# Kernel tuning notes

Measured on AMD Instinct MI355X. Metric: run time of the kernel, lower is better.

Reference implementation:

```python
import jax, jax.numpy as jnp
import numpy as np

EMBED_DIM = 1024
NUM_HEADS = 16
HEAD_DIM = EMBED_DIM // NUM_HEADS


def setup_inputs() -> dict:
    key = jax.random.key(0)
    ks = jax.random.split(key, 6)
    std = 0.02
    x = jax.random.normal(ks[0], (2, 2048, EMBED_DIM), dtype=jnp.float32)
    Wq = jax.random.normal(ks[1], (EMBED_DIM, EMBED_DIM), dtype=jnp.float32) * std
    Wk = jax.random.normal(ks[2], (EMBED_DIM, EMBED_DIM), dtype=jnp.float32) * std
    Wv = jax.random.normal(ks[3], (EMBED_DIM, EMBED_DIM), dtype=jnp.float32) * std
    Wo = jax.random.normal(ks[4], (EMBED_DIM, EMBED_DIM), dtype=jnp.float32) * std
    Wf = jax.random.normal(ks[5], (NUM_HEADS, EMBED_DIM), dtype=jnp.float32) * std
    return {"x": x, "Wq": Wq, "Wk": Wk, "Wv": Wv, "Wo": Wo, "Wf": Wf}


def reference(x, Wq, Wk, Wv, Wo, Wf):
    b, n, d = x.shape
    h, hd = NUM_HEADS, HEAD_DIM
    # projections (nn.Linear without bias: y = x @ W^T)
    q = (x @ Wq.T).reshape(b, n, h, hd)
    k = (x @ Wk.T).reshape(b, n, h, hd)
    v = (x @ Wv.T).reshape(b, n, h, hd)
    # per-head log forget gate and its causal cumulative sum
    log_f = jax.nn.log_sigmoid(x @ Wf.T)          # [b, n, h]
    c = jnp.cumsum(log_f, axis=1)                 # [b, n, h], c_i = sum_{t<=i} log f_t
    cbh = c.transpose(0, 2, 1)                    # [b, h, n]
    scale = 1.0 / np.sqrt(hd).astype(np.float32)
    # scores s_ij = q_i.k_j * scale + (c_i - c_j)  (decay D_ij = sum_{t=j+1}^i log f_t)
    scores = jnp.einsum("bihd,bjhd->bhij", q, k) * scale
    scores = scores + cbh[:, :, :, None] - cbh[:, :, None, :]
    causal = jnp.tril(jnp.ones((n, n), dtype=bool))
    scores = jnp.where(causal, scores, -1e30)
    p = jax.nn.softmax(scores, axis=-1)           # [b, h, n, n]
    out = jnp.einsum("bhij,bjhd->bihd", p, v).reshape(b, n, d)
    return out @ Wo.T
```

## Files before the change

### kernel.cpp

```cpp
#include <hip/hip_runtime.h>

#define EMBED 1024
#define NHEAD 16
#define HD    64
#define SEQ   2048
#define BATCH 2
#define ROWS  (BATCH * SEQ)

typedef float f32x4 __attribute__((ext_vector_type(4)));
typedef short short8 __attribute__((ext_vector_type(8)));
typedef short short4v __attribute__((ext_vector_type(4)));
typedef unsigned short u16x4 __attribute__((ext_vector_type(4)));
typedef unsigned short u16x8 __attribute__((ext_vector_type(8)));
typedef unsigned u32x4 __attribute__((ext_vector_type(4)));
typedef unsigned u32x2 __attribute__((ext_vector_type(2)));

#define LOG2E 1.4426950408889634f

__device__ __forceinline__ unsigned short f2bf(float f) {
  unsigned int u = __builtin_bit_cast(unsigned int, f);
  u += 0x7fffu + ((u >> 16) & 1u);
  return (unsigned short)(u >> 16);
}

__device__ __forceinline__ unsigned cvtpk(float lo, float hi) {
  unsigned r;
  asm("v_cvt_pk_bf16_f32 %0, %1, %2" : "=v"(r) : "v"(lo), "v"(hi));
  return r;
}

#if __has_builtin(__builtin_amdgcn_exp2f)
#define EXP2(x) __builtin_amdgcn_exp2f(x)
#else
#define EXP2(x) exp2f(x)
#endif

__device__ __forceinline__ void gll16(const void* g, const void* l) {
  __builtin_amdgcn_global_load_lds(
      (const __attribute__((address_space(1))) unsigned int*)g,
      (__attribute__((address_space(3))) unsigned int*)l, 16, 0, 0);
}

__device__ __forceinline__ unsigned lds_addr(const void* p) {
  return (unsigned)(size_t)(__attribute__((address_space(3))) const void*)p;
}

__global__ __launch_bounds__(256) void cvt_all_kernel(
    const float* __restrict__ x,
    const float* __restrict__ w0, const float* __restrict__ w1,
    const float* __restrict__ w2, const float* __restrict__ w3,
    const float* __restrict__ wf,
    unsigned short* __restrict__ xo,
    unsigned short* __restrict__ o0, unsigned short* __restrict__ o1,
    unsigned short* __restrict__ o2, unsigned short* __restrict__ o3,
    unsigned short* __restrict__ wfh, unsigned short* __restrict__ wfl,
    unsigned* __restrict__ qkmaxu) {
  const int y = blockIdx.y;
  if (y < 4) {
    const float* in = (y == 0) ? w0 : (y == 1) ? w1 : (y == 2) ? w2 : w3;
    unsigned short* out = (y == 0) ? o0 : (y == 1) ? o1 : (y == 2) ? o2 : o3;
    const int i = blockIdx.x * 256 + threadIdx.x;
    f32x4 v = reinterpret_cast<const f32x4*>(in)[i];
    u16x4 o;
#pragma unroll
    for (int e = 0; e < 4; ++e) o[e] = f2bf(v[e]);
    reinterpret_cast<u16x4*>(out)[i] = o;
  } else if (y == 4) {
    const int i0 = blockIdx.x * 256 + threadIdx.x;
#pragma unroll
    for (int e = 0; e < 4; ++e) {
      const int i = i0 + e * 262144;
      f32x4 v = reinterpret_cast<const f32x4*>(x)[i];
      u16x4 h;
#pragma unroll
      for (int q = 0; q < 4; ++q) h[q] = f2bf(v[q]);
      reinterpret_cast<u16x4*>(xo)[i] = h;
    }
  } else {
    if (blockIdx.x < 16) {
      const int i = blockIdx.x * 256 + threadIdx.x;
      f32x4 v = reinterpret_cast<const f32x4*>(wf)[i];
      u16x4 h, l;
#pragma unroll
      for (int q = 0; q < 4; ++q) {
        h[q] = f2bf(v[q]);
        const float hf = __builtin_bit_cast(float, (unsigned)h[q] << 16);
        l[q] = f2bf(v[q] - hf);
      }
      reinterpret_cast<u16x4*>(wfh)[i] = h;
      reinterpret_cast<u16x4*>(wfl)[i] = l;
    } else if (blockIdx.x == 16) {
      if (threadIdx.x < 64) qkmaxu[threadIdx.x] = 0u;
    }
  }
}

__global__ __launch_bounds__(256) void gemm_wo_kernel(
    const unsigned short* __restrict__ A, const unsigned short* __restrict__ B,
    float* __restrict__ C) {
  __shared__ unsigned short Asm[64 * 64];
  __shared__ unsigned short Bsm[128 * 64];
  const int tid = threadIdx.x, wid = tid >> 6, lane = tid & 63;
  const int g = lane >> 4, l16 = lane & 15;
  const int wr = wid >> 1, wc = wid & 1;
  const int mb = blockIdx.y;
  const int nb = blockIdx.x;

  f32x4 acc[2][4] = {};

  for (int k0 = 0; k0 < EMBED; k0 += 64) {
    __syncthreads();
#pragma unroll
    for (int q = 0; q < 2; ++q) {
      const int base = (wid * 2 + q) * 1024;
      const int off = base + lane * 16;
      const int row = off >> 7;
      const int colel = (off & 127) >> 1;
      gll16(A + (size_t)(mb * 64 + row) * EMBED + k0 + colel, (const char*)Asm + base);
    }
#pragma unroll
    for (int q = 0; q < 4; ++q) {
      const int base = (wid * 4 + q) * 1024;
      const int off = base + lane * 16;
      const int row = off >> 7;
      const int colel = (off & 127) >> 1;
      gll16(B + (size_t)(nb * 128 + row) * EMBED + k0 + colel, (const char*)Bsm + base);
    }
    __syncthreads();

#pragma unroll
    for (int kc = 0; kc < 2; ++kc) {
      short8 am[2], bm[4];
#pragma unroll
      for (int mi = 0; mi < 2; ++mi)
        am[mi] = *reinterpret_cast<const short8*>(&Asm[(wr * 32 + mi * 16 + l16) * 64 + kc * 32 + g * 8]);
#pragma unroll
      for (int ni = 0; ni < 4; ++ni)
        bm[ni] = *reinterpret_cast<const short8*>(&Bsm[(wc * 64 + ni * 16 + l16) * 64 + kc * 32 + g * 8]);
#pragma unroll
      for (int mi = 0; mi < 2; ++mi)
#pragma unroll
        for (int ni = 0; ni < 4; ++ni)
          acc[mi][ni] = __builtin_amdgcn_mfma_f32_16x16x32_bf16(am[mi], bm[ni], acc[mi][ni], 0, 0, 0);
    }
  }

#pragma unroll
  for (int mi = 0; mi < 2; ++mi)
#pragma unroll
    for (int ni = 0; ni < 4; ++ni)
#pragma unroll
      for (int r = 0; r < 4; ++r) {
        const int m = mb * 64 + wr * 32 + mi * 16 + g * 4 + r;
        const int n = nb * 128 + wc * 64 + ni * 16 + l16;
        C[(size_t)m * EMBED + n] = acc[mi][ni][r];
      }
}

#define BAR() asm volatile("s_barrier" ::: "memory")
#define LGKM0()                                              \
  do {                                                       \
    asm volatile("s_waitcnt lgkmcnt(0)" ::: "memory");       \
    __builtin_amdgcn_sched_barrier(0);                       \
  } while (0)
#define VM(n_) asm volatile("s_waitcnt vmcnt(" #n_ ")" ::: "memory")

template <bool OUT_BF16>
__global__ __launch_bounds__(512, 2) void gemm256_kernel(
    const unsigned short* __restrict__ A,
    const unsigned short* __restrict__ B0, const unsigned short* __restrict__ B1,
    const unsigned short* __restrict__ B2,
    void* __restrict__ C0, void* __restrict__ C1, void* __restrict__ C2,
    unsigned* __restrict__ qkmaxu) {
  __shared__ unsigned short sm[2][2][2][8192];
  const int tid = threadIdx.x, wid = tid >> 6, lane = tid & 63;
  const int g = lane >> 4, l16 = lane & 15;
  const int wr = wid >> 2, wcol = wid & 3;
  const int mb = blockIdx.y;
  const int nb = blockIdx.x;
  const int which = nb >> 2;
  const int col0 = (nb & 3) * 256;
  const unsigned short* Bp = (which == 0) ? B0 : (which == 1) ? B1 : B2;
  void* Cp = (which == 0) ? C0 : (which == 1) ? C1 : C2;

  const int lane8 = lane & 7, laneHi = lane >> 3;
  const int colel = (lane8 ^ laneHi) * 8;
  int soff[2];
#pragma unroll
  for (int q = 0; q < 2; ++q)
    soff[q] = (q * 64 + wid * 8 + laneHi) * EMBED + colel;
  const unsigned short* Ag = A + (size_t)(mb * 256) * EMBED;
  const unsigned short* Bg = Bp + (size_t)col0 * EMBED;

  const int sw = (l16 & 7) << 4;
  const int cs0 = (0 | (g * 16)) ^ sw;
  const int cs1 = (64 | (g * 16)) ^ sw;
  const char* smB = (const char*)sm;
  const int aBase = wr * 16384 + l16 * 128;
  const int bBase = 32768 + (wcol >> 1) * 16384 + (wcol & 1) * 8192 + l16 * 128;

#define STG(buf_, ab_, half_, gsrc_, t_)                                               \
  do {                                                                                 \
    const unsigned short* gp_ = (gsrc_) + (size_t)(half_) * (128 * EMBED) + (t_) * 64; \
    char* lp_ = (char*)sm + (buf_) * 65536 + (ab_) * 32768 + (half_) * 16384 + wid * 1024; \
    gll16(gp_ + soff[0], lp_);                                                         \
    gll16(gp_ + soff[1], lp_ + 8192);                                                  \
  } while (0)

#define RD_A(buf_, row_, kc_) \
  (*reinterpret_cast<const short8*>(smB + (buf_) * 65536 + aBase + (row_) * 2048 + ((kc_) ? cs1 : cs0)))
#define RD_B(buf_, row_, kc_) \
  (*reinterpret_cast<const short8*>(smB + (buf_) * 65536 + bBase + (row_) * 2048 + ((kc_) ? cs1 : cs0)))

#define QUAD(mg_, ng_)                                                                   \
  do {                                                                                   \
    __builtin_amdgcn_s_setprio(1);                                                       \
    _Pragma("unroll") for (int kc_ = 0; kc_ < 2; ++kc_)                                  \
      _Pragma("unroll") for (int mi_ = 0; mi_ < 4; ++mi_)                                \
        _Pragma("unroll") for (int nj_ = 0; nj_ < 2; ++nj_)                              \
          acc[(mg_) * 4 + mi_][(ng_) * 2 + nj_] = __builtin_amdgcn_mfma_f32_16x16x32_bf16( \
              fa[mi_][kc_], fb[(ng_) * 2 + nj_][kc_], acc[(mg_) * 4 + mi_][(ng_) * 2 + nj_], 0, 0, 0); \
    __builtin_amdgcn_s_setprio(0);                                                       \
  } while (0)

#define KTILE4(BUF_, STG_P1, STG_P2, STG_P3, STG_P4_VM)                                  \
  do {                                                                                   \
    _Pragma("unroll") for (int mi_ = 0; mi_ < 4; ++mi_) {                                \
      fa[mi_][0] = RD_A(BUF_, mi_, 0);                                                   \
      fa[mi_][1] = RD_A(BUF_, mi_, 1);                                                   \
    }                                                                                    \
    _Pragma("unroll") for (int ni_ = 0; ni_ < 2; ++ni_) {                                \
      fb[ni_][0] = RD_B(BUF_, ni_, 0);                                                   \
      fb[ni_][1] = RD_B(BUF_, ni_, 1);                                                   \
    }                                                                                    \
    STG_P1;                                                                              \
    asm volatile("s_waitcnt lgkmcnt(8)" ::: "memory");                                   \
    BAR();                                                                               \
    LGKM0();                                                                             \
    QUAD(0, 0);                                                                          \
    BAR();                                                                               \
    _Pragma("unroll") for (int ni_ = 0; ni_ < 2; ++ni_) {                                \
      fb[2 + ni_][0] = RD_B(BUF_, 2 + ni_, 0);                                           \
      fb[2 + ni_][1] = RD_B(BUF_, 2 + ni_, 1);                                           \
    }                                                                                    \
    STG_P2;                                                                              \
    BAR();                                                                               \
    LGKM0();                                                                             \
    QUAD(0, 1);                                                                          \
    BAR();                                                                               \
    _Pragma("unroll") for (int mi_ = 0; mi_ < 4; ++mi_) {                                \
      fa[mi_][0] = RD_A(BUF_, 4 + mi_, 0);                                               \
      fa[mi_][1] = RD_A(BUF_, 4 + mi_, 1);                                               \
    }                                                                                    \
    STG_P3;                                                                              \
    BAR();                                                                               \
    LGKM0();                                                                             \
    QUAD(1, 0);                                                                          \
    BAR();                                                                               \
    STG_P4_VM;                                                                           \
    BAR();                                                                               \
    QUAD(1, 1);                                                                          \
    BAR();                                                                               \
  } while (0)

  short8 fa[4][2], fb[4][2];
  f32x4 acc[8][4] = {};

  STG(0, 0, 0, Ag, 0);
  STG(0, 1, 0, Bg, 0);
  STG(0, 0, 1, Ag, 0);
  STG(0, 1, 1, Bg, 0);
  STG(1, 1, 0, Bg, 1);
  STG(1, 1, 1, Bg, 1);
  VM(4);
  BAR();

  for (int it = 0; it < 8; ++it) {
    const int t1 = 2 * it + 1, t2 = 2 * it + 2, t3 = 2 * it + 3;
    const bool nl = (it < 7);
    KTILE4(0,
           STG(1, 0, 0, Ag, t1),
           STG(1, 0, 1, Ag, t1),
           if (nl) STG(0, 1, 0, Bg, t2),
           if (nl) { STG(0, 1, 1, Bg, t2); VM(4); } else VM(0));
    KTILE4(1,
           if (nl) STG(0, 0, 0, Ag, t2),
           if (nl) STG(0, 0, 1, Ag, t2),
           if (nl) STG(1, 1, 0, Bg, t3),
           if (nl) { STG(1, 1, 1, Bg, t3); VM(4); });
  }

  unsigned mxv = 0;
#pragma unroll
  for (int mi = 0; mi < 8; ++mi)
#pragma unroll
    for (int ni = 0; ni < 4; ++ni)
#pragma unroll
      for (int r = 0; r < 4; ++r) {
        const int m = mb * 256 + wr * 128 + mi * 16 + g * 4 + r;
        const int n = col0 + wcol * 64 + ni * 16 + l16;
        if (OUT_BF16) {
          const unsigned short bv = f2bf(acc[mi][ni][r]);
          ((unsigned short*)Cp)[(size_t)m * EMBED + n] = bv;
          const unsigned a = bv & 0x7fffu;
          mxv = a > mxv ? a : mxv;
        } else {
          ((float*)Cp)[(size_t)m * EMBED + n] = acc[mi][ni][r];
        }
      }
  if (OUT_BF16 && which < 2) {
#pragma unroll
    for (int mm = 1; mm < 64; mm <<= 1) {
      const unsigned o = __shfl_xor(mxv, mm);
      mxv = o > mxv ? o : mxv;
    }
    if (lane == 0) {
      const int bbat = (mb >= 8) ? 1 : 0;
      const int head = (nb & 3) * 4 + wcol;
      const int idx = which * 32 + bbat * 16 + head;
      atomicMax(&qkmaxu[idx], mxv << 16);
    }
  }
#undef STG
#undef RD_A
#undef RD_B
#undef QUAD
#undef KTILE4
}
#undef BAR
#undef LGKM0
#undef VM

__global__ __launch_bounds__(256) void gate_kernel(
    const float* __restrict__ x,
    const unsigned short* __restrict__ wh, const unsigned short* __restrict__ wl,
    float* __restrict__ c) {
  __shared__ f32x4 red[4][64];
  const int tid = threadIdx.x, wid = tid >> 6, lane = tid & 63;
  const int g = lane >> 4, l16 = lane & 15;
  const int row0 = blockIdx.x * 16;
  const int k0 = wid * 256;
  const float* xp = x + (size_t)(row0 + l16) * EMBED + k0 + g * 8;
  const unsigned short* whp = wh + (size_t)l16 * EMBED + k0 + g * 8;
  const unsigned short* wlp = wl + (size_t)l16 * EMBED + k0 + g * 8;
  f32x4 acc = {};
#pragma unroll
  for (int k = 0; k < 8; ++k) {
    const f32x4 v0 = *reinterpret_cast<const f32x4*>(xp + k * 32);
    const f32x4 v1 = *reinterpret_cast<const f32x4*>(xp + k * 32 + 4);
    short8 ah, al;
#pragma unroll
    for (int e = 0; e < 4; ++e) {
      const unsigned short h0 = f2bf(v0[e]);
      ah[e] = (short)h0;
      al[e] = (short)f2bf(v0[e] - __builtin_bit_cast(float, (unsigned)h0 << 16));
      const unsigned short h1 = f2bf(v1[e]);
      ah[e + 4] = (short)h1;
      al[e + 4] = (short)f2bf(v1[e] - __builtin_bit_cast(float, (unsigned)h1 << 16));
    }
    const short8 bh = *reinterpret_cast<const short8*>(whp + k * 32);
    const short8 bl = *reinterpret_cast<const short8*>(wlp + k * 32);
    acc = __builtin_amdgcn_mfma_f32_16x16x32_bf16(ah, bh, acc, 0, 0, 0);
    acc = __builtin_amdgcn_mfma_f32_16x16x32_bf16(ah, bl, acc, 0, 0, 0);
    acc = __builtin_amdgcn_mfma_f32_16x16x32_bf16(al, bh, acc, 0, 0, 0);
  }
  red[wid][lane] = acc;
  __syncthreads();
  if (wid == 0) {
    const f32x4 a = red[0][lane] + red[1][lane] + red[2][lane] + red[3][lane];
#pragma unroll
    for (int r = 0; r < 4; ++r) {
      const float s = a[r];
      const float ls = (fminf(s, 0.f) - log1pf(__expf(-fabsf(s)))) * LOG2E;
      const int n = row0 + g * 4 + r;
      const int b = n >> 11, nn = n & (SEQ - 1);
      c[(size_t)(b * NHEAD + l16) * SEQ + nn] = ls;
    }
  }
}

__global__ void cumsum_kernel(float* __restrict__ c) {
  const int bh = blockIdx.x;
  const int lane = threadIdx.x;
  float* p = c + (size_t)bh * SEQ;
  f32x4 vv[8];
  f32x4* vp = reinterpret_cast<f32x4*>(p + lane * 32);
#pragma unroll
  for (int q = 0; q < 8; ++q) vv[q] = vp[q];
  float run = 0.f;
#pragma unroll
  for (int q = 0; q < 8; ++q)
#pragma unroll
    for (int e = 0; e < 4; ++e) { run += vv[q][e]; vv[q][e] = run; }
  float s = run;
#pragma unroll
  for (int off = 1; off < 64; off <<= 1) {
    float u = __shfl_up(s, off);
    if (lane >= off) s += u;
  }
  const float excl = s - run;
#pragma unroll
  for (int q = 0; q < 8; ++q)
#pragma unroll
    for (int e = 0; e < 4; ++e) vv[q][e] += excl;
#pragma unroll
  for (int q = 0; q < 8; ++q) vp[q] = vv[q];
}

#define NINF (-3.0e38f)
#define SCL (0.125f * LOG2E)
#define BMARG 14.0f

#define TR_READ(dst, addr, OFF) \
  asm volatile("ds_read_b64_tr_b16 %0, %1 offset:" OFF : "=v"(dst) : "v"(addr))

__global__ __launch_bounds__(256) void fa_attn_kernel(
    const unsigned short* __restrict__ Q, const unsigned short* __restrict__ K,
    const unsigned short* __restrict__ V, const float* __restrict__ C,
    const float* __restrict__ qkmax, unsigned short* __restrict__ O) {
  __shared__ unsigned short Ksm[2][4096];
  __shared__ unsigned short Vsm[2][4096];
  const int p = blockIdx.x;
  const int xcd = p & 7, s2 = p >> 3;
  const int hb = xcd * 4 + (s2 >> 5);
  const int qb = s2 & 31;
  const int hh = hb & 15, bb = hb >> 4;
  const int tid = threadIdx.x, wid = tid >> 6, lane = tid & 63;
  const int g = lane >> 4, l16 = lane & 15;
  const int i_base = qb * 64 + wid * 16;

  const float* cptr = C + (size_t)(bb * NHEAD + hh) * SEQ;

  int kOff[2], vOff[2];
#pragma unroll
  for (int qq = 0; qq < 2; ++qq) {
    const int q = wid * 2 + qq;
    {
      const int row = q * 8 + (lane >> 3);
      const int colel = ((lane & 7) ^ (lane >> 3)) * 8;
      kOff[qq] = row * EMBED + colel;
    }
    {
      const int dblk = q >> 1;
      const int j = (q & 1) * 32 + (lane >> 1);
      const int dlow = (lane & 1) * 8;
      vOff[qq] = j * EMBED + dblk * 16 + dlow;
    }
  }
  const unsigned short* Kbase = K + (size_t)bb * SEQ * EMBED + hh * HD;
  const unsigned short* Vbase = V + (size_t)bb * SEQ * EMBED + hh * HD;

  const int swz = (l16 & 7) << 4;
  const int koffB0 = ((0) | (g * 16)) ^ swz;
  const int koffB1 = ((64) | (g * 16)) ^ swz;
  const int krowB = l16 * 128;

#define STAGE(bufidx, tt)                                                              \
  do {                                                                                 \
    const unsigned short* kb_ = Kbase + (size_t)(tt) * 64 * EMBED;                     \
    const unsigned short* vb_ = Vbase + (size_t)(tt) * 64 * EMBED;                     \
    _Pragma("unroll") for (int qq = 0; qq < 2; ++qq) {                                 \
      gll16(kb_ + kOff[qq], (const char*)&Ksm[bufidx][0] + (wid * 2 + qq) * 1024);     \
      gll16(vb_ + vOff[qq], (const char*)&Vsm[bufidx][0] + (wid * 2 + qq) * 1024);     \
    }                                                                                  \
  } while (0)

  short8 qf0, qf1;
  {
    const unsigned short* qp = Q + (size_t)(bb * SEQ + i_base + l16) * EMBED + hh * HD + g * 8;
    qf0 = *reinterpret_cast<const short8*>(qp);
    qf1 = *reinterpret_cast<const short8*>(qp + 32);
  }
  const float c2i = cptr[i_base + l16];

  int t_start = qb;
  {
    const float qm = qkmax[hb];
    const float km = qkmax[32 + hb];
    const float thr = -41.f - 23.0832f * qm * km;
    const float c2imin = cptr[qb * 64];
    while (t_start > 0 && (c2imin - cptr[t_start * 64 - 1] >= thr)) --t_start;
  }

  float mc_prev = (t_start == qb) ? c2i : cptr[t_start * 64 + 63];
  float l_ = 0.f;
  f32x4 accd[4] = {};

  STAGE(0, t_start);
  __syncthreads();

  int buf = 0;
  for (int t = t_start; t <= qb; ++t) {
    if (t < qb) STAGE(buf ^ 1, t + 1);
    const int kv0 = t * 64;
    const bool diag = (t == qb);
    const int nj = diag ? (wid + 1) : 4;

    const float mc_cur = diag ? c2i : cptr[kv0 + 63];
    const float corr = EXP2(mc_cur - mc_prev);
    mc_prev = mc_cur;
    const float mcB = mc_cur - BMARG;

    float pf[4][4];
    float lsum = 0.f;
#pragma unroll
    for (int jb = 0; jb < 4; ++jb) {
      if (jb < nj) {
        const char* kbp = (const char*)&Ksm[buf][0] + jb * 2048 + krowB;
        short8 kf0 = *reinterpret_cast<const short8*>(kbp + koffB0);
        short8 kf1 = *reinterpret_cast<const short8*>(kbp + koffB1);
        f32x4 s = {};
        __builtin_amdgcn_s_setprio(1);
        s = __builtin_amdgcn_mfma_f32_16x16x32_bf16(kf0, qf0, s, 0, 0, 0);
        s = __builtin_amdgcn_mfma_f32_16x16x32_bf16(kf1, qf1, s, 0, 0, 0);
        __builtin_amdgcn_s_setprio(0);
        const f32x4 cv = *reinterpret_cast<const f32x4*>(&cptr[kv0 + jb * 16 + g * 4]);
#pragma unroll
        for (int r = 0; r < 4; ++r) {
          float arg = __builtin_fmaf(s[r], SCL, mcB - cv[r]);
          if (diag && jb == wid && (g * 4 + r > l16)) arg = NINF;
          const float pv = EXP2(arg);
          pf[jb][r] = pv;
          lsum += pv;
        }
      } else {
#pragma unroll
        for (int r = 0; r < 4; ++r) pf[jb][r] = 0.f;
      }
    }
    l_ = l_ * corr + lsum;
#pragma unroll
    for (int d = 0; d < 4; ++d) accd[d] *= corr;

    u32x4 w0, w1;
    w0[0] = cvtpk(pf[0][0], pf[0][1]); w0[1] = cvtpk(pf[0][2], pf[0][3]);
    w0[2] = cvtpk(pf[1][0], pf[1][1]); w0[3] = cvtpk(pf[1][2], pf[1][3]);
    w1[0] = cvtpk(pf[2][0], pf[2][1]); w1[1] = cvtpk(pf[2][2], pf[2][3]);
    w1[2] = cvtpk(pf[3][0], pf[3][1]); w1[3] = cvtpk(pf[3][2], pf[3][3]);
    const short8 pb0 = __builtin_bit_cast(short8, w0);
    const short8 pb1 = __builtin_bit_cast(short8, w1);

    const unsigned vb0 = lds_addr(&Vsm[buf][0]) + lane * 8;
#pragma unroll
    for (int db = 0; db < 4; ++db) {
      const unsigned va = vb0 + db * 2048;
      short4v t0, t1, t2, t3;
      TR_READ(t0, va, "0");
      TR_READ(t1, va, "512");
      TR_READ(t2, va, "1024");
      TR_READ(t3, va, "1536");
      asm volatile("s_waitcnt lgkmcnt(0)" ::: "memory");
      __builtin_amdgcn_sched_barrier(0);
      short8 va0, va1;
#pragma unroll
      for (int e = 0; e < 4; ++e) {
        va0[e] = t0[e]; va0[e + 4] = t1[e];
        va1[e] = t2[e]; va1[e + 4] = t3[e];
      }
      __builtin_amdgcn_s_setprio(1);
      accd[db] = __builtin_amdgcn_mfma_f32_16x16x32_bf16(va0, pb0, accd[db], 0, 0, 0);
      accd[db] = __builtin_amdgcn_mfma_f32_16x16x32_bf16(va1, pb1, accd[db], 0, 0, 0);
      __builtin_amdgcn_s_setprio(0);
    }
    __syncthreads();
    buf ^= 1;
  }

  l_ += __shfl_xor(l_, 16);
  l_ += __shfl_xor(l_, 32);
  const float inv = 1.0f / l_;
  unsigned short* op = O + (size_t)(bb * SEQ + i_base + l16) * EMBED + hh * HD;
#pragma unroll
  for (int db = 0; db < 4; ++db) {
    u32x2 o;
    o[0] = cvtpk(accd[db][0] * inv, accd[db][1] * inv);
    o[1] = cvtpk(accd[db][2] * inv, accd[db][3] * inv);
    *reinterpret_cast<u32x2*>(op + db * 16 + g * 4) = o;
  }
#undef STAGE
}

extern "C" void kernel_launch(void* const* d_in, const int* in_sizes, int n_in,
                              void* d_out, int out_size, void* d_ws, size_t ws_size,
                              hipStream_t stream) {
  const float* x = (const float*)d_in[0];
  const float* Wq = (const float*)d_in[1];
  const float* Wk = (const float*)d_in[2];
  const float* Wv = (const float*)d_in[3];
  const float* Wo = (const float*)d_in[4];
  const float* Wf = (const float*)d_in[5];
  float* out = (float*)d_out;

  char* ws = (char*)d_ws;
  const size_t SZ_X = (size_t)ROWS * EMBED * sizeof(unsigned short);
  const size_t SZ_W = (size_t)EMBED * EMBED * sizeof(unsigned short);
  const size_t SZ_WF = (size_t)NHEAD * EMBED * sizeof(unsigned short);
  unsigned short* xb = (unsigned short*)ws;   ws += SZ_X;
  unsigned short* Wqb = (unsigned short*)ws;  ws += SZ_W;
  unsigned short* Wkb = (unsigned short*)ws;  ws += SZ_W;
  unsigned short* Wvb = (unsigned short*)ws;  ws += SZ_W;
  unsigned short* Wob = (unsigned short*)ws;  ws += SZ_W;
  unsigned short* Wfh = (unsigned short*)ws;  ws += SZ_WF;
  unsigned short* Wfl = (unsigned short*)ws;  ws += SZ_WF;
  unsigned short* Qb = (unsigned short*)ws;   ws += SZ_X;
  unsigned short* Kb = (unsigned short*)ws;   ws += SZ_X;
  unsigned short* Vb = (unsigned short*)ws;   ws += SZ_X;
  unsigned short* attnb = (unsigned short*)ws; ws += SZ_X;
  float* carr = (float*)ws;                   ws += (size_t)BATCH * NHEAD * SEQ * sizeof(float);
  float* qkmax = (float*)ws;                  ws += 64 * sizeof(float);

  cvt_all_kernel<<<dim3(1024, 6), 256, 0, stream>>>(
      x, Wq, Wk, Wv, Wo, Wf, xb, Wqb, Wkb, Wvb, Wob, Wfh, Wfl,
      (unsigned*)qkmax);

  gate_kernel<<<256, 256, 0, stream>>>(x, Wfh, Wfl, carr);

  gemm256_kernel<true><<<dim3(12, 16), 512, 0, stream>>>(
      xb, Wqb, Wkb, Wvb, Qb, Kb, Vb, (unsigned*)qkmax);

  cumsum_kernel<<<BATCH * NHEAD, 64, 0, stream>>>(carr);

  fa_attn_kernel<<<1024, 256, 0, stream>>>(Qb, Kb, Vb, carr, qkmax, attnb);

  gemm_wo_kernel<<<dim3(8, 64), 256, 0, stream>>>(attnb, Wob, out);
}
```

Baseline: 97.74 us.

## Fuse forget-gate projection into QKV GEMM launch as extra blocks

Removes the separate gate kernel and runs its work in 64 extra blocks appended to the QKV GEMM grid, which becomes a 1D grid of 256 blocks. Each of these blocks has 8 waves covering 4 row tiles with a two-way K split, and reduces the halves through shared memory. The aim is to save one kernel launch and let the gate work fill CUs the 192 GEMM blocks leave idle on the 256-CU device. The cost is that the GEMM kernel gets more code and possibly more register pressure, and the gate blocks use a 512-thread configuration.

Measured after the change: 89.80 us. 1.09x faster.

```diff
diff --git a/kernel.cpp b/kernel.cpp
--- a/kernel.cpp
+++ b/kernel.cpp
@@ -165,23 +165,72 @@
   } while (0)
 #define VM(n_) asm volatile("s_waitcnt vmcnt(" #n_ ")" ::: "memory")
 
-template <bool OUT_BF16>
 __global__ __launch_bounds__(512, 2) void gemm256_kernel(
     const unsigned short* __restrict__ A,
     const unsigned short* __restrict__ B0, const unsigned short* __restrict__ B1,
     const unsigned short* __restrict__ B2,
-    void* __restrict__ C0, void* __restrict__ C1, void* __restrict__ C2,
-    unsigned* __restrict__ qkmaxu) {
+    unsigned short* __restrict__ C0, unsigned short* __restrict__ C1,
+    unsigned short* __restrict__ C2, unsigned* __restrict__ qkmaxu,
+    const float* __restrict__ x, const unsigned short* __restrict__ wfh,
+    const unsigned short* __restrict__ wfl, float* __restrict__ carr) {
   __shared__ unsigned short sm[2][2][2][8192];
   const int tid = threadIdx.x, wid = tid >> 6, lane = tid & 63;
   const int g = lane >> 4, l16 = lane & 15;
+
+  if (blockIdx.x >= 192) {
+    const int bid2 = blockIdx.x - 192;
+    const int tile = bid2 * 4 + (wid >> 1);
+    const int half = wid & 1;
+    const int row0 = tile * 16;
+    const int k0 = half * 512;
+    const float* xp = x + (size_t)(row0 + l16) * EMBED + k0 + g * 8;
+    const unsigned short* whp = wfh + (size_t)l16 * EMBED + k0 + g * 8;
+    const unsigned short* wlp = wfl + (size_t)l16 * EMBED + k0 + g * 8;
+    f32x4 acc = {};
+#pragma unroll
+    for (int k = 0; k < 16; ++k) {
+      const f32x4 v0 = *reinterpret_cast<const f32x4*>(xp + k * 32);
+      const f32x4 v1 = *reinterpret_cast<const f32x4*>(xp + k * 32 + 4);
+      short8 ah, al;
+#pragma unroll
+      for (int e = 0; e < 4; ++e) {
+        const unsigned short h0 = f2bf(v0[e]);
+        ah[e] = (short)h0;
+        al[e] = (short)f2bf(v0[e] - __builtin_bit_cast(float, (unsigned)h0 << 16));
+        const unsigned short h1 = f2bf(v1[e]);
+        ah[e + 4] = (short)h1;
+        al[e + 4] = (short)f2bf(v1[e] - __builtin_bit_cast(float, (unsigned)h1 << 16));
+      }
+      const short8 bh = *reinterpret_cast<const short8*>(whp + k * 32);
+      const short8 bl = *reinterpret_cast<const short8*>(wlp + k * 32);
+      acc = __builtin_amdgcn_mfma_f32_16x16x32_bf16(ah, bh, acc, 0, 0, 0);
+      acc = __builtin_amdgcn_mfma_f32_16x16x32_bf16(ah, bl, acc, 0, 0, 0);
+      acc = __builtin_amdgcn_mfma_f32_16x16x32_bf16(al, bh, acc, 0, 0, 0);
+    }
+    f32x4* red = reinterpret_cast<f32x4*>(sm);
+    red[wid * 64 + lane] = acc;
+    __syncthreads();
+    if (half == 0) {
+      const f32x4 a = red[wid * 64 + lane] + red[(wid + 1) * 64 + lane];
+#pragma unroll
+      for (int r = 0; r < 4; ++r) {
+        const float s = a[r];
+        const float ls = (fminf(s, 0.f) - log1pf(__expf(-fabsf(s)))) * LOG2E;
+        const int n = row0 + g * 4 + r;
+        const int b = n >> 11, nn = n & (SEQ - 1);
+        carr[(size_t)(b * NHEAD + l16) * SEQ + nn] = ls;
+      }
+    }
+    return;
+  }
+
   const int wr = wid >> 2, wcol = wid & 3;
-  const int mb = blockIdx.y;
-  const int nb = blockIdx.x;
+  const int mb = blockIdx.x / 12;
+  const int nb = blockIdx.x % 12;
   const int which = nb >> 2;
   const int col0 = (nb & 3) * 256;
   const unsigned short* Bp = (which == 0) ? B0 : (which == 1) ? B1 : B2;
-  void* Cp = (which == 0) ? C0 : (which == 1) ? C1 : C2;
+  unsigned short* Cp = (which == 0) ? C0 : (which == 1) ? C1 : C2;
 
   const int lane8 = lane & 7, laneHi = lane >> 3;
   const int colel = (lane8 ^ laneHi) * 8;
@@ -299,16 +348,12 @@
       for (int r = 0; r < 4; ++r) {
         const int m = mb * 256 + wr * 128 + mi * 16 + g * 4 + r;
         const int n = col0 + wcol * 64 + ni * 16 + l16;
-        if (OUT_BF16) {
-          const unsigned short bv = f2bf(acc[mi][ni][r]);
-          ((unsigned short*)Cp)[(size_t)m * EMBED + n] = bv;
-          const unsigned a = bv & 0x7fffu;
-          mxv = a > mxv ? a : mxv;
-        } else {
-          ((float*)Cp)[(size_t)m * EMBED + n] = acc[mi][ni][r];
-        }
+        const unsigned short bv = f2bf(acc[mi][ni][r]);
+        Cp[(size_t)m * EMBED + n] = bv;
+        const unsigned a = bv & 0x7fffu;
+        mxv = a > mxv ? a : mxv;
       }
-  if (OUT_BF16 && which < 2) {
+  if (which < 2) {
 #pragma unroll
     for (int mm = 1; mm < 64; mm <<= 1) {
       const unsigned o = __shfl_xor(mxv, mm);
@@ -330,54 +375,6 @@
 #undef BAR
 #undef LGKM0
 #undef VM
-
-__global__ __launch_bounds__(256) void gate_kernel(
-    const float* __restrict__ x,
-    const unsigned short* __restrict__ wh, const unsigned short* __restrict__ wl,
-    float* __restrict__ c) {
-  __shared__ f32x4 red[4][64];
-  const int tid = threadIdx.x, wid = tid >> 6, lane = tid & 63;
-  const int g = lane >> 4, l16 = lane & 15;
-  const int row0 = blockIdx.x * 16;
-  const int k0 = wid * 256;
-  const float* xp = x + (size_t)(row0 + l16) * EMBED + k0 + g * 8;
-  const unsigned short* whp = wh + (size_t)l16 * EMBED + k0 + g * 8;
-  const unsigned short* wlp = wl + (size_t)l16 * EMBED + k0 + g * 8;
-  f32x4 acc = {};
-#pragma unroll
-  for (int k = 0; k < 8; ++k) {
-    const f32x4 v0 = *reinterpret_cast<const f32x4*>(xp + k * 32);
-    const f32x4 v1 = *reinterpret_cast<const f32x4*>(xp + k * 32 + 4);
-    short8 ah, al;
-#pragma unroll
-    for (int e = 0; e < 4; ++e) {
-      const unsigned short h0 = f2bf(v0[e]);
-      ah[e] = (short)h0;
-      al[e] = (short)f2bf(v0[e] - __builtin_bit_cast(float, (unsigned)h0 << 16));
-      const unsigned short h1 = f2bf(v1[e]);
-      ah[e + 4] = (short)h1;
-      al[e + 4] = (short)f2bf(v1[e] - __builtin_bit_cast(float, (unsigned)h1 << 16));
-    }
-    const short8 bh = *reinterpret_cast<const short8*>(whp + k * 32);
-    const short8 bl = *reinterpret_cast<const short8*>(wlp + k * 32);
-    acc = __builtin_amdgcn_mfma_f32_16x16x32_bf16(ah, bh, acc, 0, 0, 0);
-    acc = __builtin_amdgcn_mfma_f32_16x16x32_bf16(ah, bl, acc, 0, 0, 0);
-    acc = __builtin_amdgcn_mfma_f32_16x16x32_bf16(al, bh, acc, 0, 0, 0);
-  }
-  red[wid][lane] = acc;
-  __syncthreads();
-  if (wid == 0) {
-    const f32x4 a = red[0][lane] + red[1][lane] + red[2][lane] + red[3][lane];
-#pragma unroll
-    for (int r = 0; r < 4; ++r) {
-      const float s = a[r];
-      const float ls = (fminf(s, 0.f) - log1pf(__expf(-fabsf(s)))) * LOG2E;
-      const int n = row0 + g * 4 + r;
-      const int b = n >> 11, nn = n & (SEQ - 1);
-      c[(size_t)(b * NHEAD + l16) * SEQ + nn] = ls;
-    }
-  }
-}
 
 __global__ void cumsum_kernel(float* __restrict__ c) {
   const int bh = blockIdx.x;
@@ -613,10 +610,8 @@
       x, Wq, Wk, Wv, Wo, Wf, xb, Wqb, Wkb, Wvb, Wob, Wfh, Wfl,
       (unsigned*)qkmax);
 
-  gate_kernel<<<256, 256, 0, stream>>>(x, Wfh, Wfl, carr);
-
-  gemm256_kernel<true><<<dim3(12, 16), 512, 0, stream>>>(
-      xb, Wqb, Wkb, Wvb, Qb, Kb, Vb, (unsigned*)qkmax);
+  gemm256_kernel<<<256, 512, 0, stream>>>(
+      xb, Wqb, Wkb, Wvb, Qb, Kb, Vb, (unsigned*)qkmax, x, Wfh, Wfl, carr);
 
   cumsum_kernel<<<BATCH * NHEAD, 64, 0, stream>>>(carr);
 
```
